# Performance work log

Hardware: AMD Instinct MI355X
Metric: run time of the kernel (lower is better)

## Reference

```python
import jax, jax.numpy as jnp
import numpy as np

B, S, H, F, E, K = 2, 2048, 1024, 4096, 8, 2


def setup_inputs() -> dict:
    key = jax.random.key(0)
    ks = jax.random.split(key, 5)
    scale = 0.02
    return {
        "hidden_states": jax.random.normal(ks[0], (B, S, H), jnp.float32),
        "gate_w": jax.random.normal(ks[1], (H, E), jnp.float32) * scale,  # nn.Linear(H,E,bias=False)
        "w1": jax.random.normal(ks[2], (E, H, F), jnp.float32) * scale,   # per-expert fc1
        "b1": jnp.zeros((E, F), jnp.float32),
        "w2": jax.random.normal(ks[3], (E, F, H), jnp.float32) * scale,   # per-expert fc2
        "b2": jnp.zeros((E, H), jnp.float32),
    }


def reference(hidden_states, gate_w, w1, b1, w2, b2):
    b, s, h = hidden_states.shape
    x = hidden_states.reshape(b * s, h)  # [T, H]
    T = x.shape[0]
    n_experts = gate_w.shape[1]

    # --- Top-K gating ---
    router_logits = x @ gate_w                      # [T, E]
    router_probs = jax.nn.softmax(router_logits, axis=-1)
    topk_probs, topk_idx = jax.lax.top_k(router_probs, K)  # [T, K]
    topk_probs = topk_probs / topk_probs.sum(axis=-1, keepdims=True)
    aux_loss = n_experts * jnp.sum(router_probs.mean(axis=0) ** 2)

    # --- Combine weights: scatter normalized top-k probs into dense [T, E] ---
    combine_w = jnp.zeros((T, n_experts), x.dtype).at[
        jnp.arange(T)[:, None], topk_idx
    ].add(topk_probs)

    # --- Expert MLPs (dense per-expert batched GEMM; zero combine weight drops unrouted) ---
    hidden = jax.nn.relu(jnp.einsum('th,ehf->etf', x, w1) + b1[:, None, :])  # [E, T, F]
    expert_out = jnp.einsum('etf,efh->eth', hidden, w2) + b2[:, None, :]     # [E, T, H]

    out = jnp.einsum('te,eth->th', combine_w, expert_out)  # weighted combine
    return out.reshape(b, s, h), aux_loss
```

## Files before the change

kernel.cpp:

```cpp
#include <hip/hip_runtime.h>
#include <hip/hip_bf16.h>
#include <cstdint>

#define AS1 __attribute__((address_space(1)))
#define AS3 __attribute__((address_space(3)))

typedef __attribute__((ext_vector_type(8))) short short8x;
typedef __attribute__((ext_vector_type(4))) float f32x4;

static constexpr int T    = 4096;
static constexpr int HD   = 1024;
static constexpr int FD   = 4096;
static constexpr int NE   = 8;
static constexpr int P    = T * 2;
static constexpr int PPAD = P + 128;
static constexpr int MAXTILES = P / 128 + NE;
static constexpr int RTB  = 16;
static constexpr int RNB  = T / RTB;

struct TileDesc { int e; int start; int rows; int pad; };

__device__ __forceinline__ uint16_t f2bf(float f) {
  uint32_t u = __builtin_bit_cast(uint32_t, f);
  u += 0x7FFFu + ((u >> 16) & 1u);
  return (uint16_t)(u >> 16);
}
__device__ __forceinline__ float bf2f(uint16_t b) {
  uint32_t u = ((uint32_t)b) << 16;
  return __builtin_bit_cast(float, u);
}

__device__ __forceinline__ void gload_lds16(const void* g, void* l) {
  __builtin_amdgcn_global_load_lds((const AS1 uint32_t*)g, (AS3 uint32_t*)l, 16, 0, 0);
}

__global__ __launch_bounds__(256) void cvt_x_kernel(const float* __restrict__ x,
                                                    uint16_t* __restrict__ xb) {
  size_t i = ((size_t)blockIdx.x * 256 + threadIdx.x) * 4;
  float4 v = *(const float4*)&x[i];
  ushort4 o;
  o.x = f2bf(v.x); o.y = f2bf(v.y); o.z = f2bf(v.z); o.w = f2bf(v.w);
  *(ushort4*)&xb[i] = o;
}

__global__ __launch_bounds__(256) void transpose_cvt_kernel(
    const float* __restrict__ in, uint16_t* __restrict__ out, int R, int C) {
  __shared__ float tile[64][65];
  int z = blockIdx.z;
  const float* inp = in + (size_t)z * R * C;
  uint16_t* outp = out + (size_t)z * R * C;
  int r0 = blockIdx.y * 64, c0 = blockIdx.x * 64;
  int tid = threadIdx.x;
  int lr = tid >> 4;
  int lc4 = (tid & 15) * 4;
#pragma unroll
  for (int p = 0; p < 4; ++p) {
    float4 v = *(const float4*)&inp[(size_t)(r0 + lr + p * 16) * C + c0 + lc4];
    tile[lr + p * 16][lc4 + 0] = v.x;
    tile[lr + p * 16][lc4 + 1] = v.y;
    tile[lr + p * 16][lc4 + 2] = v.z;
    tile[lr + p * 16][lc4 + 3] = v.w;
  }
  __syncthreads();
#pragma unroll
  for (int p = 0; p < 4; ++p) {
    int c = lr + p * 16;
    ushort4 o;
    o.x = f2bf(tile[lc4 + 0][c]);
    o.y = f2bf(tile[lc4 + 1][c]);
    o.z = f2bf(tile[lc4 + 2][c]);
    o.w = f2bf(tile[lc4 + 3][c]);
    *(ushort4*)&outp[(size_t)(c0 + c) * R + r0 + lc4] = o;
  }
}

__global__ __launch_bounds__(256) void router_kernel(
    const float* __restrict__ x, const float* __restrict__ gate_w,
    int* __restrict__ topk_idx, float* __restrict__ topk_w,
    float* __restrict__ part_sums, int* __restrict__ part_counts) {
  __shared__ float g[NE * HD];
  __shared__ float ls[NE];
  __shared__ int   lc[NE];
  int tid = threadIdx.x;
  for (int i = tid; i < NE * HD; i += 256)
    g[(i & 7) * HD + (i >> 3)] = gate_w[i];
  if (tid < NE) { ls[tid] = 0.f; lc[tid] = 0; }
  __syncthreads();
  int wave = tid >> 6, lane = tid & 63;
  float psum[NE];
#pragma unroll
  for (int e = 0; e < NE; ++e) psum[e] = 0.f;

  for (int tt = 0; tt < RTB / 4; ++tt) {
    int t = blockIdx.x * RTB + wave * (RTB / 4) + tt;
    const float* xr = x + (size_t)t * HD;
    float acc[NE];
#pragma unroll
    for (int e = 0; e < NE; ++e) acc[e] = 0.f;
    for (int i = 0; i < HD / 64; ++i) {
      float xv = xr[lane + i * 64];
#pragma unroll
      for (int e = 0; e < NE; ++e) acc[e] += xv * g[e * HD + lane + i * 64];
    }
#pragma unroll
    for (int off = 32; off > 0; off >>= 1)
#pragma unroll
      for (int e = 0; e < NE; ++e) acc[e] += __shfl_down(acc[e], off);
    if (lane == 0) {
      float m = acc[0];
#pragma unroll
      for (int e = 1; e < NE; ++e) m = fmaxf(m, acc[e]);
      float p[NE], s = 0.f;
#pragma unroll
      for (int e = 0; e < NE; ++e) { p[e] = expf(acc[e] - m); s += p[e]; }
      float inv = 1.f / s;
#pragma unroll
      for (int e = 0; e < NE; ++e) { p[e] *= inv; psum[e] += p[e]; }
      int i0 = 0;
#pragma unroll
      for (int e = 1; e < NE; ++e) if (p[e] > p[i0]) i0 = e;
      int i1 = (i0 == 0) ? 1 : 0;
#pragma unroll
      for (int e = 0; e < NE; ++e) if (e != i0 && e != i1 && p[e] > p[i1]) i1 = e;
      float wsum = p[i0] + p[i1];
      topk_idx[t * 2] = i0; topk_idx[t * 2 + 1] = i1;
      topk_w[t * 2] = p[i0] / wsum; topk_w[t * 2 + 1] = p[i1] / wsum;
      atomicAdd(&lc[i0], 1); atomicAdd(&lc[i1], 1);
    }
  }
  if (lane == 0)
#pragma unroll
    for (int e = 0; e < NE; ++e) atomicAdd(&ls[e], psum[e]);
  __syncthreads();
  if (tid < NE) {
    part_sums[blockIdx.x * NE + tid]   = ls[tid];
    part_counts[blockIdx.x * NE + tid] = lc[tid];
  }
}

__global__ __launch_bounds__(64) void finalize_kernel(
    const int* __restrict__ part_counts, const float* __restrict__ part_sums,
    int* __restrict__ offsets, TileDesc* __restrict__ desc,
    int* __restrict__ ntiles, float* __restrict__ aux_out) {
  __shared__ int   csh[NE];
  __shared__ float ssh[NE];
  int tid = threadIdx.x;
  if (tid < NE) {
    int c = 0; float s = 0.f;
    for (int b = 0; b < RNB; ++b) {
      c += part_counts[b * NE + tid];
      s += part_sums[b * NE + tid];
    }
    csh[tid] = c; ssh[tid] = s;
  }
  __syncthreads();
  if (tid == 0) {
    int off = 0, nt = 0;
    for (int e = 0; e < NE; ++e) {
      offsets[e] = off;
      int c = csh[e];
      for (int i = 0; i < c; i += 128) {
        int rows = c - i; if (rows > 128) rows = 128;
        desc[nt].e = e; desc[nt].start = off + i; desc[nt].rows = rows; desc[nt].pad = 0;
        nt++;
      }
      off += c;
    }
    *ntiles = nt;
    float aux = 0.f;
    for (int e = 0; e < NE; ++e) {
      float mean = ssh[e] / (float)T;
      aux += mean * mean;
    }
    *aux_out = (float)NE * aux;
  }
}

__global__ __launch_bounds__(256) void scatter_kernel(
    const int* __restrict__ topk_idx, const int* __restrict__ offsets,
    int* __restrict__ fill, int* __restrict__ pair_tok, int* __restrict__ tok_pos) {
  int t = blockIdx.x * 256 + threadIdx.x;
  int lane = threadIdx.x & 63;
  unsigned long long below = (lane == 63) ? ~0ull >> 1
                                          : ((1ull << (lane + 1)) - 1) >> 1;
#pragma unroll
  for (int k = 0; k < 2; ++k) {
    int e = topk_idx[t * 2 + k];
    int pos = 0;
    for (int ex = 0; ex < NE; ++ex) {
      unsigned long long m = __ballot(e == ex);
      if (e == ex) {
        int leader = __ffsll((long long)m) - 1;
        int cnt = __popcll(m);
        int base = 0;
        if (lane == leader) base = atomicAdd(&fill[ex], cnt);
        base = __shfl(base, leader);
        pos = base + __popcll(m & below);
      }
    }
    int pp = offsets[e] + pos;
    pair_tok[pp] = t;
    tok_pos[t * 2 + k] = pp;
  }
}

template <int KD, int ND, int EPI>
__global__ __launch_bounds__(256) void moe_gemm(
    const uint16_t* __restrict__ Abase, const int* __restrict__ pair_tok,
    const uint16_t* __restrict__ Bw, const float* __restrict__ bias,
    uint16_t* __restrict__ Cout, const TileDesc* __restrict__ desc,
    const int* __restrict__ ntiles) {
  constexpr int NB = ND / 128;
  constexpr int TOTAL = NB * MAXTILES;
  constexpr int SM = 8;

  int orig = blockIdx.x;
  int work = (orig & 7) * (TOTAL / 8) + (orig >> 3);
  int srow = work / (SM * NB);
  int rem  = work % (SM * NB);
  int nb   = rem / SM;
  int mt   = srow * SM + (rem & (SM - 1));

  if (mt >= *ntiles) return;
  TileDesc d = desc[mt];

  __shared__ uint16_t As[2][128 * 32];
  __shared__ uint16_t Bs[2][128 * 32];
  __shared__ int rowA[128];

  int tid = threadIdx.x, lane = tid & 63, wave = tid >> 6;
  int wm = wave >> 1, wn = wave & 1;

  int idx0 = (wave * 2 + 0) * 64 + lane;
  int idx1 = (wave * 2 + 1) * 64 + lane;
  int ar0 = idx0 >> 2, kc0 = idx0 & 3;
  int ar1 = idx1 >> 2, kc1 = idx1 & 3;

  int ra0, ra1;
  if constexpr (EPI == 0) {
    if (tid < 128) rowA[tid] = (tid < d.rows) ? pair_tok[d.start + tid] : 0;
    __syncthreads();
    ra0 = rowA[ar0]; ra1 = rowA[ar1];
  } else {
    ra0 = d.start + ar0; ra1 = d.start + ar1;
  }

  const uint16_t* Bbase = Bw + ((size_t)d.e * ND + (size_t)nb * 128) * KD;
  const uint16_t* Arow0 = Abase + (size_t)ra0 * KD + kc0 * 8;
  const uint16_t* Arow1 = Abase + (size_t)ra1 * KD + kc1 * 8;
  const uint16_t* Brow0 = Bbase + (size_t)ar0 * KD + kc0 * 8;
  const uint16_t* Brow1 = Bbase + (size_t)ar1 * KD + kc1 * 8;

  auto stage = [&](int buf, int kt) {
    int kb = kt * 32;
    gload_lds16(Arow0 + kb, &As[buf][(wave * 2 + 0) * 512]);
    gload_lds16(Arow1 + kb, &As[buf][(wave * 2 + 1) * 512]);
    gload_lds16(Brow0 + kb, &Bs[buf][(wave * 2 + 0) * 512]);
    gload_lds16(Brow1 + kb, &Bs[buf][(wave * 2 + 1) * 512]);
  };

  f32x4 acc[4][4];
#pragma unroll
  for (int i = 0; i < 4; ++i)
#pragma unroll
    for (int j = 0; j < 4; ++j) acc[i][j] = (f32x4){0.f, 0.f, 0.f, 0.f};

  constexpr int NT = KD / 32;
  stage(0, 0);
  __syncthreads();

  for (int kt = 0; kt < NT; ++kt) {
    int cur = kt & 1;
    if (kt + 1 < NT) stage(cur ^ 1, kt + 1);

    short8x af[4], bfr[4];
#pragma unroll
    for (int i = 0; i < 4; ++i)
      af[i] = *(const short8x*)&As[cur][(wm * 64 + i * 16 + (lane & 15)) * 32 + (lane >> 4) * 8];
#pragma unroll
    for (int j = 0; j < 4; ++j)
      bfr[j] = *(const short8x*)&Bs[cur][(wn * 64 + j * 16 + (lane & 15)) * 32 + (lane >> 4) * 8];
#pragma unroll
    for (int i = 0; i < 4; ++i)
#pragma unroll
      for (int j = 0; j < 4; ++j)
        acc[i][j] = __builtin_amdgcn_mfma_f32_16x16x32_bf16(af[i], bfr[j], acc[i][j], 0, 0, 0);

    __syncthreads();
  }

  int rq = (lane >> 4) * 4;
  int cl = lane & 15;
#pragma unroll
  for (int i = 0; i < 4; ++i) {
    int rb = wm * 64 + i * 16 + rq;
#pragma unroll
    for (int j = 0; j < 4; ++j) {
      int col = nb * 128 + wn * 64 + j * 16 + cl;
      float bv = bias[d.e * ND + col];
#pragma unroll
      for (int q = 0; q < 4; ++q) {
        int r = rb + q;
        if (r < d.rows) {
          float v = acc[i][j][q] + bv;
          if (EPI == 0) v = fmaxf(v, 0.f);
          Cout[(size_t)(d.start + r) * ND + col] = f2bf(v);
        }
      }
    }
  }
}

__global__ __launch_bounds__(256) void combine_kernel(
    const uint16_t* __restrict__ po, const int* __restrict__ tok_pos,
    const float* __restrict__ topk_w, float* __restrict__ out) {
  int t = blockIdx.x;
  int c = threadIdx.x * 4;
  int p0 = tok_pos[t * 2], p1 = tok_pos[t * 2 + 1];
  float w0 = topk_w[t * 2], w1 = topk_w[t * 2 + 1];
  ushort4 a = *(const ushort4*)&po[(size_t)p0 * HD + c];
  ushort4 b = *(const ushort4*)&po[(size_t)p1 * HD + c];
  float4 o;
  o.x = w0 * bf2f(a.x) + w1 * bf2f(b.x);
  o.y = w0 * bf2f(a.y) + w1 * bf2f(b.y);
  o.z = w0 * bf2f(a.z) + w1 * bf2f(b.z);
  o.w = w0 * bf2f(a.w) + w1 * bf2f(b.w);
  *(float4*)&out[(size_t)t * HD + c] = o;
}

extern "C" void kernel_launch(void* const* d_in, const int* in_sizes, int n_in,
                              void* d_out, int out_size, void* d_ws, size_t ws_size,
                              hipStream_t stream) {
  const float* x      = (const float*)d_in[0];
  const float* gate_w = (const float*)d_in[1];
  const float* w1     = (const float*)d_in[2];
  const float* b1     = (const float*)d_in[3];
  const float* w2     = (const float*)d_in[4];
  const float* b2     = (const float*)d_in[5];
  float* out = (float*)d_out;
  (void)in_sizes; (void)n_in; (void)out_size; (void)ws_size;

  char* w = (char*)d_ws;
  size_t off = 0;
  auto alloc = [&](size_t bytes) -> void* {
    void* p = w + off;
    off = (off + bytes + 255) & ~(size_t)255;
    return p;
  };
  int*      meta     = (int*)alloc(256);
  int*      fill     = meta;
  int*      offsets  = (int*)alloc(256);
  int*      ntiles   = offsets + 8;
  TileDesc* desc     = (TileDesc*)alloc(sizeof(TileDesc) * 128);
  int*      topk_idx = (int*)alloc(sizeof(int) * P);
  float*    topk_w   = (float*)alloc(sizeof(float) * P);
  int*      tok_pos  = (int*)alloc(sizeof(int) * P);
  int*      pair_tok = (int*)alloc(sizeof(int) * PPAD);
  float*    psums    = (float*)alloc(sizeof(float) * RNB * NE);
  int*      pcounts  = (int*)alloc(sizeof(int) * RNB * NE);
  uint16_t* xb       = (uint16_t*)alloc((size_t)T * HD * 2);
  uint16_t* w1t      = (uint16_t*)alloc((size_t)NE * FD * HD * 2);
  uint16_t* w2t      = (uint16_t*)alloc((size_t)NE * HD * FD * 2);
  uint16_t* hidden   = (uint16_t*)alloc((size_t)PPAD * FD * 2);
  uint16_t* pout     = (uint16_t*)alloc((size_t)PPAD * HD * 2);

  hipMemsetAsync(meta, 0, 256, stream);
  cvt_x_kernel<<<(T * HD) / 1024, 256, 0, stream>>>(x, xb);
  transpose_cvt_kernel<<<dim3(FD / 64, HD / 64, NE), 256, 0, stream>>>(w1, w1t, HD, FD);
  transpose_cvt_kernel<<<dim3(HD / 64, FD / 64, NE), 256, 0, stream>>>(w2, w2t, FD, HD);
  router_kernel<<<RNB, 256, 0, stream>>>(x, gate_w, topk_idx, topk_w, psums, pcounts);
  finalize_kernel<<<1, 64, 0, stream>>>(pcounts, psums, offsets, desc, ntiles,
                                        out + (size_t)T * HD);
  scatter_kernel<<<T / 256, 256, 0, stream>>>(topk_idx, offsets, fill, pair_tok, tok_pos);
  moe_gemm<HD, FD, 0><<<(FD / 128) * MAXTILES, 256, 0, stream>>>(
      xb, pair_tok, w1t, b1, hidden, desc, ntiles);
  moe_gemm<FD, HD, 1><<<(HD / 128) * MAXTILES, 256, 0, stream>>>(
      hidden, pair_tok, w2t, b2, pout, desc, ntiles);
  combine_kernel<<<T, 256, 0, stream>>>(pout, tok_pos, topk_w, out);
}
```

Baseline: 422.2 us.

## Rewrite expert GEMMs with 256x256 tiles, swizzled LDS and ping-pong MFMA schedule

```diff
diff --git a/kernel.cpp b/kernel.cpp
--- a/kernel.cpp
+++ b/kernel.cpp
@@ -4,6 +4,7 @@
 
 #define AS1 __attribute__((address_space(1)))
 #define AS3 __attribute__((address_space(3)))
+#define SBAR() asm volatile("s_barrier" ::: "memory")
 
 typedef __attribute__((ext_vector_type(8))) short short8x;
 typedef __attribute__((ext_vector_type(4))) float f32x4;
@@ -13,8 +14,8 @@
 static constexpr int FD   = 4096;
 static constexpr int NE   = 8;
 static constexpr int P    = T * 2;
-static constexpr int PPAD = P + 128;
-static constexpr int MAXTILES = P / 128 + NE;
+static constexpr int PPAD = P + 256;
+static constexpr int MAXT256 = P / 256 + NE;
 static constexpr int RTB  = 16;
 static constexpr int RNB  = T / RTB;
 
@@ -32,6 +33,12 @@
 
 __device__ __forceinline__ void gload_lds16(const void* g, void* l) {
   __builtin_amdgcn_global_load_lds((const AS1 uint32_t*)g, (AS3 uint32_t*)l, 16, 0, 0);
+}
+
+__device__ __forceinline__ short8x ds128(uint32_t addr) {
+  short8x r;
+  asm volatile("ds_read_b128 %0, %1" : "=v"(r) : "v"(addr));
+  return r;
 }
 
 __global__ __launch_bounds__(256) void cvt_x_kernel(const float* __restrict__ x,
@@ -140,8 +147,8 @@
 
 __global__ __launch_bounds__(64) void finalize_kernel(
     const int* __restrict__ part_counts, const float* __restrict__ part_sums,
-    int* __restrict__ offsets, TileDesc* __restrict__ desc,
-    int* __restrict__ ntiles, float* __restrict__ aux_out) {
+    int* __restrict__ offsets, TileDesc* __restrict__ desc256,
+    int* __restrict__ ntiles256, float* __restrict__ aux_out) {
   __shared__ int   csh[NE];
   __shared__ float ssh[NE];
   int tid = threadIdx.x;
@@ -155,18 +162,18 @@
   }
   __syncthreads();
   if (tid == 0) {
-    int off = 0, nt = 0;
+    int off = 0, nt2 = 0;
     for (int e = 0; e < NE; ++e) {
       offsets[e] = off;
       int c = csh[e];
-      for (int i = 0; i < c; i += 128) {
-        int rows = c - i; if (rows > 128) rows = 128;
-        desc[nt].e = e; desc[nt].start = off + i; desc[nt].rows = rows; desc[nt].pad = 0;
-        nt++;
+      for (int i = 0; i < c; i += 256) {
+        int rows = c - i; if (rows > 256) rows = 256;
+        desc256[nt2].e = e; desc256[nt2].start = off + i; desc256[nt2].rows = rows;
+        desc256[nt2].pad = 0; nt2++;
       }
       off += c;
     }
-    *ntiles = nt;
+    *ntiles256 = nt2;
     float aux = 0.f;
     for (int e = 0; e < NE; ++e) {
       float mean = ssh[e] / (float)T;
@@ -204,107 +211,181 @@
   }
 }
 
-template <int KD, int ND, int EPI>
-__global__ __launch_bounds__(256) void moe_gemm(
-    const uint16_t* __restrict__ Abase, const int* __restrict__ pair_tok,
+template <int KD, int ND, bool GATHER, bool RELU>
+__global__ __launch_bounds__(512, 2) void moe_gemm8(
+    const uint16_t* __restrict__ A, const int* __restrict__ pair_tok,
     const uint16_t* __restrict__ Bw, const float* __restrict__ bias,
-    uint16_t* __restrict__ Cout, const TileDesc* __restrict__ desc,
-    const int* __restrict__ ntiles) {
-  constexpr int NB = ND / 128;
-  constexpr int TOTAL = NB * MAXTILES;
-  constexpr int SM = 8;
+    uint16_t* __restrict__ C, const TileDesc* __restrict__ desc,
+    const int* __restrict__ nt_ptr) {
+  constexpr int NBC   = ND / 256;
+  constexpr int NT    = KD / 64;
+  constexpr int ASLOT = 16384;
+  constexpr int BOFF  = 2 * ASLOT;
+  constexpr int GRIDT = NBC * MAXT256;
+
+  extern __shared__ char smem[];
+  uint16_t* lds = (uint16_t*)smem;
+  int* rowA = (int*)(smem + 131072);
 
   int orig = blockIdx.x;
-  int work = (orig & 7) * (TOTAL / 8) + (orig >> 3);
-  int srow = work / (SM * NB);
-  int rem  = work % (SM * NB);
-  int nb   = rem / SM;
-  int mt   = srow * SM + (rem & (SM - 1));
-
-  if (mt >= *ntiles) return;
+  int work = (orig & 7) * (GRIDT / 8) + (orig >> 3);
+  int nb = work % NBC;
+  int mt = work / NBC;
+  if (mt >= *nt_ptr) return;
   TileDesc d = desc[mt];
 
-  __shared__ uint16_t As[2][128 * 32];
-  __shared__ uint16_t Bs[2][128 * 32];
-  __shared__ int rowA[128];
-
   int tid = threadIdx.x, lane = tid & 63, wave = tid >> 6;
-  int wm = wave >> 1, wn = wave & 1;
-
-  int idx0 = (wave * 2 + 0) * 64 + lane;
-  int idx1 = (wave * 2 + 1) * 64 + lane;
-  int ar0 = idx0 >> 2, kc0 = idx0 & 3;
-  int ar1 = idx1 >> 2, kc1 = idx1 & 3;
-
-  int ra0, ra1;
-  if constexpr (EPI == 0) {
-    if (tid < 128) rowA[tid] = (tid < d.rows) ? pair_tok[d.start + tid] : 0;
+  int wm = wave >> 2, wn = wave & 3;
+
+  if constexpr (GATHER) {
+    if (tid < 256) rowA[tid] = (tid < d.rows) ? pair_tok[d.start + tid] : 0;
     __syncthreads();
-    ra0 = rowA[ar0]; ra1 = rowA[ar1];
-  } else {
-    ra0 = d.start + ar0; ra1 = d.start + ar1;
-  }
-
-  const uint16_t* Bbase = Bw + ((size_t)d.e * ND + (size_t)nb * 128) * KD;
-  const uint16_t* Arow0 = Abase + (size_t)ra0 * KD + kc0 * 8;
-  const uint16_t* Arow1 = Abase + (size_t)ra1 * KD + kc1 * 8;
-  const uint16_t* Brow0 = Bbase + (size_t)ar0 * KD + kc0 * 8;
-  const uint16_t* Brow1 = Bbase + (size_t)ar1 * KD + kc1 * 8;
-
-  auto stage = [&](int buf, int kt) {
-    int kb = kt * 32;
-    gload_lds16(Arow0 + kb, &As[buf][(wave * 2 + 0) * 512]);
-    gload_lds16(Arow1 + kb, &As[buf][(wave * 2 + 1) * 512]);
-    gload_lds16(Brow0 + kb, &Bs[buf][(wave * 2 + 0) * 512]);
-    gload_lds16(Brow1 + kb, &Bs[buf][(wave * 2 + 1) * 512]);
+  }
+
+  int wl8 = wave * 8 + (lane >> 3);
+  int colel = (((lane & 7) ^ (lane >> 3)) << 3);
+  const uint16_t* Asrc[4];
+  const uint16_t* Bsrc[4];
+#pragma unroll
+  for (int i = 0; i < 4; ++i) {
+    int r = i * 64 + wl8;
+    int gr;
+    if constexpr (GATHER) gr = rowA[r]; else gr = d.start + r;
+    Asrc[i] = A + (size_t)gr * KD + colel;
+    Bsrc[i] = Bw + ((size_t)d.e * ND + nb * 256 + r) * KD + colel;
+  }
+
+  auto stage = [&](int slot, int kt) {
+    int ko = kt * 64;
+#pragma unroll
+    for (int i = 0; i < 4; ++i)
+      gload_lds16(Asrc[i] + ko, &lds[slot * ASLOT + i * 4096 + wave * 512]);
+#pragma unroll
+    for (int j = 0; j < 4; ++j)
+      gload_lds16(Bsrc[j] + ko, &lds[BOFF + slot * ASLOT + j * 4096 + wave * 512]);
   };
 
-  f32x4 acc[4][4];
-#pragma unroll
-  for (int i = 0; i < 4; ++i)
+  uint32_t ldsu = (uint32_t)(uintptr_t)(AS3 char*)smem;
+  int rd0 = (lane & 15) * 64 + ((((lane >> 4)) ^ (lane & 7)) << 3);
+  int rd1 = (lane & 15) * 64 + ((((lane >> 4) | 4) ^ (lane & 7)) << 3);
+  uint32_t aA0 = ldsu + (uint32_t)(wm * 8192 + rd0) * 2;
+  uint32_t aA1 = ldsu + (uint32_t)(wm * 8192 + rd1) * 2;
+  uint32_t aB0 = ldsu + (uint32_t)(BOFF + wn * 4096 + rd0) * 2;
+  uint32_t aB1 = ldsu + (uint32_t)(BOFF + wn * 4096 + rd1) * 2;
+
+  f32x4 acc[8][4];
+#pragma unroll
+  for (int i = 0; i < 8; ++i)
 #pragma unroll
     for (int j = 0; j < 4; ++j) acc[i][j] = (f32x4){0.f, 0.f, 0.f, 0.f};
 
-  constexpr int NT = KD / 32;
+  short8x aq[4][2], bA[2][2], bB[2][2];
+
   stage(0, 0);
-  __syncthreads();
+  stage(1, 1);
+  asm volatile("s_waitcnt vmcnt(8)" ::: "memory");
+  SBAR();
 
   for (int kt = 0; kt < NT; ++kt) {
-    int cur = kt & 1;
-    if (kt + 1 < NT) stage(cur ^ 1, kt + 1);
-
-    short8x af[4], bfr[4];
-#pragma unroll
-    for (int i = 0; i < 4; ++i)
-      af[i] = *(const short8x*)&As[cur][(wm * 64 + i * 16 + (lane & 15)) * 32 + (lane >> 4) * 8];
-#pragma unroll
-    for (int j = 0; j < 4; ++j)
-      bfr[j] = *(const short8x*)&Bs[cur][(wn * 64 + j * 16 + (lane & 15)) * 32 + (lane >> 4) * 8];
-#pragma unroll
-    for (int i = 0; i < 4; ++i)
-#pragma unroll
-      for (int j = 0; j < 4; ++j)
-        acc[i][j] = __builtin_amdgcn_mfma_f32_16x16x32_bf16(af[i], bfr[j], acc[i][j], 0, 0, 0);
-
-    __syncthreads();
-  }
-
-  int rq = (lane >> 4) * 4;
-  int cl = lane & 15;
-#pragma unroll
-  for (int i = 0; i < 4; ++i) {
-    int rb = wm * 64 + i * 16 + rq;
-#pragma unroll
-    for (int j = 0; j < 4; ++j) {
-      int col = nb * 128 + wn * 64 + j * 16 + cl;
-      float bv = bias[d.e * ND + col];
+    int slot = kt & 1;
+    uint32_t sa = slot ? 32768u : 0u;
+
+#pragma unroll
+    for (int fm = 0; fm < 4; ++fm) {
+      aq[fm][0] = ds128(aA0 + sa + fm * 2048);
+      aq[fm][1] = ds128(aA1 + sa + fm * 2048);
+    }
+#pragma unroll
+    for (int fn = 0; fn < 2; ++fn) {
+      bA[fn][0] = ds128(aB0 + sa + fn * 2048);
+      bA[fn][1] = ds128(aB1 + sa + fn * 2048);
+    }
+    SBAR();
+    asm volatile("s_waitcnt lgkmcnt(0)" ::: "memory");
+    __builtin_amdgcn_sched_barrier(0);
+    __builtin_amdgcn_s_setprio(1);
+#pragma unroll
+    for (int fm = 0; fm < 4; ++fm)
+#pragma unroll
+      for (int fn = 0; fn < 2; ++fn) {
+        acc[fm][fn] = __builtin_amdgcn_mfma_f32_16x16x32_bf16(aq[fm][0], bA[fn][0], acc[fm][fn], 0, 0, 0);
+        acc[fm][fn] = __builtin_amdgcn_mfma_f32_16x16x32_bf16(aq[fm][1], bA[fn][1], acc[fm][fn], 0, 0, 0);
+      }
+    __builtin_amdgcn_s_setprio(0);
+    SBAR();
+
+#pragma unroll
+    for (int fn = 0; fn < 2; ++fn) {
+      bB[fn][0] = ds128(aB0 + sa + (fn + 2) * 2048);
+      bB[fn][1] = ds128(aB1 + sa + (fn + 2) * 2048);
+    }
+    SBAR();
+    asm volatile("s_waitcnt lgkmcnt(0)" ::: "memory");
+    __builtin_amdgcn_sched_barrier(0);
+    __builtin_amdgcn_s_setprio(1);
+#pragma unroll
+    for (int fm = 0; fm < 4; ++fm)
+#pragma unroll
+      for (int fn = 0; fn < 2; ++fn) {
+        acc[fm][fn + 2] = __builtin_amdgcn_mfma_f32_16x16x32_bf16(aq[fm][0], bB[fn][0], acc[fm][fn + 2], 0, 0, 0);
+        acc[fm][fn + 2] = __builtin_amdgcn_mfma_f32_16x16x32_bf16(aq[fm][1], bB[fn][1], acc[fm][fn + 2], 0, 0, 0);
+      }
+    __builtin_amdgcn_s_setprio(0);
+    SBAR();
+
+#pragma unroll
+    for (int fm = 0; fm < 4; ++fm) {
+      aq[fm][0] = ds128(aA0 + sa + 8192 + fm * 2048);
+      aq[fm][1] = ds128(aA1 + sa + 8192 + fm * 2048);
+    }
+    SBAR();
+    asm volatile("s_waitcnt lgkmcnt(0)" ::: "memory");
+    __builtin_amdgcn_sched_barrier(0);
+    __builtin_amdgcn_s_setprio(1);
+#pragma unroll
+    for (int fm = 0; fm < 4; ++fm)
+#pragma unroll
+      for (int fn = 0; fn < 2; ++fn) {
+        acc[fm + 4][fn + 2] = __builtin_amdgcn_mfma_f32_16x16x32_bf16(aq[fm][0], bB[fn][0], acc[fm + 4][fn + 2], 0, 0, 0);
+        acc[fm + 4][fn + 2] = __builtin_amdgcn_mfma_f32_16x16x32_bf16(aq[fm][1], bB[fn][1], acc[fm + 4][fn + 2], 0, 0, 0);
+      }
+    __builtin_amdgcn_s_setprio(0);
+    SBAR();
+
+    bool more = (kt + 2 < NT);
+    if (more) stage(slot, kt + 2);
+    __builtin_amdgcn_s_setprio(1);
+#pragma unroll
+    for (int fm = 0; fm < 4; ++fm)
+#pragma unroll
+      for (int fn = 0; fn < 2; ++fn) {
+        acc[fm + 4][fn] = __builtin_amdgcn_mfma_f32_16x16x32_bf16(aq[fm][0], bA[fn][0], acc[fm + 4][fn], 0, 0, 0);
+        acc[fm + 4][fn] = __builtin_amdgcn_mfma_f32_16x16x32_bf16(aq[fm][1], bA[fn][1], acc[fm + 4][fn], 0, 0, 0);
+      }
+    __builtin_amdgcn_s_setprio(0);
+    if (more) asm volatile("s_waitcnt vmcnt(8)" ::: "memory");
+    else      asm volatile("s_waitcnt vmcnt(0)" ::: "memory");
+    SBAR();
+  }
+
+  int rq = (lane >> 4) * 4, cl = lane & 15;
+  float bv[4];
+#pragma unroll
+  for (int fn = 0; fn < 4; ++fn)
+    bv[fn] = bias[d.e * ND + nb * 256 + wn * 64 + fn * 16 + cl];
+#pragma unroll
+  for (int fm = 0; fm < 8; ++fm) {
+    int rb = wm * 128 + fm * 16 + rq;
+#pragma unroll
+    for (int fn = 0; fn < 4; ++fn) {
+      int col = nb * 256 + wn * 64 + fn * 16 + cl;
 #pragma unroll
       for (int q = 0; q < 4; ++q) {
         int r = rb + q;
         if (r < d.rows) {
-          float v = acc[i][j][q] + bv;
-          if (EPI == 0) v = fmaxf(v, 0.f);
-          Cout[(size_t)(d.start + r) * ND + col] = f2bf(v);
+          float v = acc[fm][fn][q] + bv[fn];
+          if constexpr (RELU) v = fmaxf(v, 0.f);
+          C[(size_t)(d.start + r) * ND + col] = f2bf(v);
         }
       }
     }
@@ -347,34 +428,36 @@
     off = (off + bytes + 255) & ~(size_t)255;
     return p;
   };
-  int*      meta     = (int*)alloc(256);
-  int*      fill     = meta;
-  int*      offsets  = (int*)alloc(256);
-  int*      ntiles   = offsets + 8;
-  TileDesc* desc     = (TileDesc*)alloc(sizeof(TileDesc) * 128);
-  int*      topk_idx = (int*)alloc(sizeof(int) * P);
-  float*    topk_w   = (float*)alloc(sizeof(float) * P);
-  int*      tok_pos  = (int*)alloc(sizeof(int) * P);
-  int*      pair_tok = (int*)alloc(sizeof(int) * PPAD);
-  float*    psums    = (float*)alloc(sizeof(float) * RNB * NE);
-  int*      pcounts  = (int*)alloc(sizeof(int) * RNB * NE);
-  uint16_t* xb       = (uint16_t*)alloc((size_t)T * HD * 2);
-  uint16_t* w1t      = (uint16_t*)alloc((size_t)NE * FD * HD * 2);
-  uint16_t* w2t      = (uint16_t*)alloc((size_t)NE * HD * FD * 2);
-  uint16_t* hidden   = (uint16_t*)alloc((size_t)PPAD * FD * 2);
-  uint16_t* pout     = (uint16_t*)alloc((size_t)PPAD * HD * 2);
+  int*      meta      = (int*)alloc(256);
+  int*      fill      = meta;
+  int*      offsets   = (int*)alloc(256);
+  int*      ntiles256 = offsets + 8;
+  TileDesc* desc256   = (TileDesc*)alloc(sizeof(TileDesc) * 64);
+  int*      topk_idx  = (int*)alloc(sizeof(int) * P);
+  float*    topk_w    = (float*)alloc(sizeof(float) * P);
+  int*      tok_pos   = (int*)alloc(sizeof(int) * P);
+  int*      pair_tok  = (int*)alloc(sizeof(int) * PPAD);
+  float*    psums     = (float*)alloc(sizeof(float) * RNB * NE);
+  int*      pcounts   = (int*)alloc(sizeof(int) * RNB * NE);
+  uint16_t* xb        = (uint16_t*)alloc((size_t)T * HD * 2);
+  uint16_t* w1t       = (uint16_t*)alloc((size_t)NE * FD * HD * 2);
+  uint16_t* w2t       = (uint16_t*)alloc((size_t)NE * HD * FD * 2);
+  uint16_t* hidden    = (uint16_t*)alloc((size_t)PPAD * FD * 2);
+  uint16_t* pout      = (uint16_t*)alloc((size_t)PPAD * HD * 2);
+
+  constexpr int GLDS = 131072 + 1024;
 
   hipMemsetAsync(meta, 0, 256, stream);
   cvt_x_kernel<<<(T * HD) / 1024, 256, 0, stream>>>(x, xb);
   transpose_cvt_kernel<<<dim3(FD / 64, HD / 64, NE), 256, 0, stream>>>(w1, w1t, HD, FD);
   transpose_cvt_kernel<<<dim3(HD / 64, FD / 64, NE), 256, 0, stream>>>(w2, w2t, FD, HD);
   router_kernel<<<RNB, 256, 0, stream>>>(x, gate_w, topk_idx, topk_w, psums, pcounts);
-  finalize_kernel<<<1, 64, 0, stream>>>(pcounts, psums, offsets, desc, ntiles,
+  finalize_kernel<<<1, 64, 0, stream>>>(pcounts, psums, offsets, desc256, ntiles256,
                                         out + (size_t)T * HD);
   scatter_kernel<<<T / 256, 256, 0, stream>>>(topk_idx, offsets, fill, pair_tok, tok_pos);
-  moe_gemm<HD, FD, 0><<<(FD / 128) * MAXTILES, 256, 0, stream>>>(
-      xb, pair_tok, w1t, b1, hidden, desc, ntiles);
-  moe_gemm<FD, HD, 1><<<(HD / 128) * MAXTILES, 256, 0, stream>>>(
-      hidden, pair_tok, w2t, b2, pout, desc, ntiles);
+  moe_gemm8<HD, FD, true, true><<<(FD / 256) * MAXT256, 512, GLDS, stream>>>(
+      xb, pair_tok, w1t, b1, hidden, desc256, ntiles256);
+  moe_gemm8<FD, HD, false, false><<<(HD / 256) * MAXT256, 512, GLDS, stream>>>(
+      hidden, nullptr, w2t, b2, pout, desc256, ntiles256);
   combine_kernel<<<T, 256, 0, stream>>>(pout, tok_pos, topk_w, out);
 }
```

Measured after the change: 417.2 us. Within noise of the previous version (-1.2%).
